# Optimization experiments

Hardware: AMD Instinct MI355X
Metric: run time of the kernel (lower is better)

The kernel has to match this reference:

```python
import jax, jax.numpy as jnp
import numpy as np

N = 100000
IN_C = 128
OUT_C = 200
E = 1600000


def gcn_conv(x, edge_index, W, b):
    """PyG GCNConv: symmetric degree-normalized aggregation with self-loops.
    out[v] = sum_{(u,v) in E+selfloops} d_u^-1/2 d_v^-1/2 (x_u @ W) + b
    """
    n = x.shape[0]
    xw = x @ W  # [N, out]
    loop = jnp.arange(n, dtype=edge_index.dtype)
    row = jnp.concatenate([edge_index[0], loop])  # src
    col = jnp.concatenate([edge_index[1], loop])  # dst
    ones = jnp.ones(row.shape[0], dtype=x.dtype)
    deg = jax.ops.segment_sum(ones, col, num_segments=n)  # in-degree incl. self
    dinv = jnp.where(deg > 0, jax.lax.rsqrt(deg), 0.0)
    norm = dinv[row] * dinv[col]  # [E+N]
    msgs = xw[row] * norm[:, None]  # [E+N, out]
    out = jax.ops.segment_sum(msgs, col, num_segments=n)
    return out + b


def setup_inputs() -> dict:
    key = jax.random.key(0)
    k1, k2, k3, k4 = jax.random.split(key, 4)
    x = jax.random.normal(k1, (N, IN_C), dtype=jnp.float32)
    edge_index = jax.random.randint(k2, (2, E), 0, N, dtype=jnp.int64)
    s1 = 1.0 / np.sqrt(IN_C)
    W1 = jax.random.uniform(k3, (IN_C, OUT_C), dtype=jnp.float32, minval=-s1, maxval=s1)
    b1 = jnp.zeros((OUT_C,), dtype=jnp.float32)
    W2 = jax.random.uniform(k4, (IN_C, OUT_C), dtype=jnp.float32, minval=-s1, maxval=s1)
    b2 = jnp.zeros((OUT_C,), dtype=jnp.float32)
    return {"x": x, "edge_index": edge_index, "W1": W1, "b1": b1, "W2": W2, "b2": b2}


def reference(x, edge_index, W1, b1, W2, b2):
    mu = gcn_conv(x, edge_index, W1, b1)
    logstd = gcn_conv(x, edge_index, W2, b2)
    return (mu, logstd)
```

## Files before the change

### kernel.cpp

```cpp
#include <hip/hip_runtime.h>

#define N_NODES 100000
#define IN_C    128
#define OUT_C   200
#define NT_TILES 13
#define KT_TILES 4

#define PSHIFT  8
#define NPB     256
#define NB      391
#define NB_POW2 512
#define BCAP    5120
#define PART_CH 4096
#define SEQ_P   16
#define SEQ_B   20

typedef __bf16 bf16_t;
typedef bf16_t bf16x8 __attribute__((ext_vector_type(8)));
typedef float  f32x4  __attribute__((ext_vector_type(4)));

__device__ __forceinline__ unsigned int bf16_bits(float f) {
    unsigned int u = __builtin_bit_cast(unsigned int, f);
    return (u + 0x7FFFu + ((u >> 16) & 1u)) >> 16;
}
__device__ __forceinline__ float bf16_lo(unsigned int p) {
    return __builtin_bit_cast(float, p << 16);
}
__device__ __forceinline__ float bf16_hi(unsigned int p) {
    return __builtin_bit_cast(float, p & 0xFFFF0000u);
}

__global__ __launch_bounds__(256) void partition_kernel(
        const int* __restrict__ row, const int* __restrict__ col, int E,
        int* __restrict__ gcount, unsigned int* __restrict__ gbuf) {
    __shared__ int hist[NB];
    __shared__ int base[NB];
    __shared__ int lofs[NB];
    __shared__ int pscan[256];
    __shared__ unsigned int stage[PART_CH];
    __shared__ unsigned short sb[PART_CH];
    const int tid = threadIdx.x;
    const int chunk = blockIdx.x * PART_CH;
    int cend = E - chunk; if (cend > PART_CH) cend = PART_CH;

    for (int i = tid; i < NB; i += 256) hist[i] = 0;
    __syncthreads();

    unsigned int   pay[SEQ_P];
    unsigned short eb[SEQ_P];
    unsigned short sq[SEQ_P];
    #pragma unroll
    for (int k = 0; k < SEQ_P; k++) {
        int i = tid + k * 256;
        eb[k] = 0xFFFFu;
        if (i < cend) {
            int c = col[chunk + i];
            int r = row[chunk + i];
            int b = (c >> PSHIFT) & (NB_POW2 - 1);
            if (b >= NB) b = NB - 1;
            pay[k] = (unsigned int)((c & (NPB - 1)) | (r << PSHIFT));
            eb[k]  = (unsigned short)b;
            sq[k]  = (unsigned short)atomicAdd(&hist[b], 1);
        }
    }
    __syncthreads();

    for (int i = tid; i < NB; i += 256)
        base[i] = atomicAdd(&gcount[i], hist[i]);

    int v0 = (2 * tid     < NB) ? hist[2 * tid]     : 0;
    int v1 = (2 * tid + 1 < NB) ? hist[2 * tid + 1] : 0;
    int s = v0 + v1;
    pscan[tid] = s;
    __syncthreads();
    for (int off = 1; off < 256; off <<= 1) {
        int u = (tid >= off) ? pscan[tid - off] : 0;
        __syncthreads();
        pscan[tid] += u;
        __syncthreads();
    }
    int ep = pscan[tid] - s;
    if (2 * tid     < NB) lofs[2 * tid]     = ep;
    if (2 * tid + 1 < NB) lofs[2 * tid + 1] = ep + v0;
    __syncthreads();

    #pragma unroll
    for (int k = 0; k < SEQ_P; k++) {
        if (eb[k] != 0xFFFFu) {
            int p = lofs[eb[k]] + sq[k];
            stage[p] = pay[k];
            sb[p] = eb[k];
        }
    }
    __syncthreads();

    for (int i = tid; i < cend; i += 256) {
        int b = sb[i];
        int p = base[b] + (i - lofs[b]);
        if (p < BCAP) gbuf[(size_t)b * BCAP + p] = stage[i];
    }
}

__global__ void bucket_scan_kernel(const int* __restrict__ gcount, int* __restrict__ gbase) {
    __shared__ int pscan[256];
    int tid = threadIdx.x;
    int v0 = (2 * tid     < NB) ? gcount[2 * tid]     : 0;
    int v1 = (2 * tid + 1 < NB) ? gcount[2 * tid + 1] : 0;
    if (v0 > BCAP) v0 = BCAP;
    if (v1 > BCAP) v1 = BCAP;
    int s = v0 + v1;
    pscan[tid] = s;
    __syncthreads();
    for (int off = 1; off < 256; off <<= 1) {
        int u = (tid >= off) ? pscan[tid - off] : 0;
        __syncthreads();
        pscan[tid] += u;
        __syncthreads();
    }
    int ep = pscan[tid] - s;
    if (2 * tid     < NB) gbase[2 * tid]     = ep;
    if (2 * tid + 1 < NB) gbase[2 * tid + 1] = ep + v0;
}

__global__ __launch_bounds__(256) void build_kernel(
        const unsigned int* __restrict__ gbuf, const int* __restrict__ gcount,
        const int* __restrict__ gbase, int* __restrict__ deg,
        int* __restrict__ offsets, float* __restrict__ dinv,
        int* __restrict__ csr_src, int n) {
    __shared__ int cnt[NPB];
    __shared__ int cur[NPB];
    __shared__ int pscan[256];
    const int b = blockIdx.x;
    const int tid = threadIdx.x;
    int total = gcount[b]; if (total > BCAP) total = BCAP;
    const int cbase = gbase[b];
    const unsigned int* bp = gbuf + (size_t)b * BCAP;

    cnt[tid] = 0;
    __syncthreads();

    unsigned int   ee[SEQ_B];
    unsigned short sq[SEQ_B];
    #pragma unroll
    for (int k = 0; k < SEQ_B; k++) {
        int i = tid + k * 256;
        ee[k] = 0xFFFFFFFFu;
        if (i < total) {
            unsigned int e = bp[i];
            ee[k] = e;
            sq[k] = (unsigned short)atomicAdd(&cnt[e & (NPB - 1)], 1);
        }
    }
    __syncthreads();

    int c = cnt[tid];
    pscan[tid] = c;
    __syncthreads();
    for (int off = 1; off < 256; off <<= 1) {
        int u = (tid >= off) ? pscan[tid - off] : 0;
        __syncthreads();
        pscan[tid] += u;
        __syncthreads();
    }
    int excl = pscan[tid] - c;
    cur[tid] = excl;
    int v = b * NPB + tid;
    if (v < n) {
        deg[v] = c;
        offsets[v] = cbase + excl;
        dinv[v] = rsqrtf((float)(c + 1));
    }
    __syncthreads();

    #pragma unroll
    for (int k = 0; k < SEQ_B; k++) {
        if (ee[k] != 0xFFFFFFFFu) {
            int p = cur[ee[k] & (NPB - 1)] + (int)sq[k];
            csr_src[cbase + p] = (int)(ee[k] >> PSHIFT);
        }
    }
}

__global__ void convert_xs_kernel(const float4* __restrict__ x, const float* __restrict__ dinv,
                                  uint2* __restrict__ xs4, int n) {
    int id = blockIdx.x * blockDim.x + threadIdx.x;
    if (id >= n * 32) return;
    int v = id >> 5;
    float dv = dinv[v];
    float4 f = x[id];
    uint2 o;
    o.x = bf16_bits(f.x * dv) | (bf16_bits(f.y * dv) << 16);
    o.y = bf16_bits(f.z * dv) | (bf16_bits(f.w * dv) << 16);
    xs4[id] = o;
}

__global__ __launch_bounds__(256) void gather_kernel(
        const uint2* __restrict__ xs4, const float* __restrict__ dinv,
        const int* __restrict__ offsets, const int* __restrict__ deg,
        const int* __restrict__ csr_src, uint2* __restrict__ agg4, int n) {
    int wave = threadIdx.x >> 6;
    int lane = threadIdx.x & 63;
    int half = lane >> 5;
    int hl   = lane & 31;
    int v = blockIdx.x * 4 + wave;
    if (v >= n) return;
    float dv = dinv[v];
    int start = offsets[v];
    int cnt = deg[v];
    float ax = 0.f, ay = 0.f, az = 0.f, aw = 0.f;

    const int* cp = csr_src + start;
    int i = 0;
    for (; i + 16 <= cnt; i += 16) {
        int u[8];
        #pragma unroll
        for (int j = 0; j < 8; j++) u[j] = __builtin_nontemporal_load(cp + i + 2 * j + half);
        uint2 t[8];
        #pragma unroll
        for (int j = 0; j < 8; j++) t[j] = xs4[(size_t)u[j] * 32 + hl];
        #pragma unroll
        for (int j = 0; j < 8; j++) {
            ax += bf16_lo(t[j].x); ay += bf16_hi(t[j].x);
            az += bf16_lo(t[j].y); aw += bf16_hi(t[j].y);
        }
    }
    if (i + 8 <= cnt) {
        int u[4];
        #pragma unroll
        for (int j = 0; j < 4; j++) u[j] = __builtin_nontemporal_load(cp + i + 2 * j + half);
        uint2 t[4];
        #pragma unroll
        for (int j = 0; j < 4; j++) t[j] = xs4[(size_t)u[j] * 32 + hl];
        #pragma unroll
        for (int j = 0; j < 4; j++) {
            ax += bf16_lo(t[j].x); ay += bf16_hi(t[j].x);
            az += bf16_lo(t[j].y); aw += bf16_hi(t[j].y);
        }
        i += 8;
    }
    if (i + 4 <= cnt) {
        int u[2];
        #pragma unroll
        for (int j = 0; j < 2; j++) u[j] = __builtin_nontemporal_load(cp + i + 2 * j + half);
        uint2 t[2];
        #pragma unroll
        for (int j = 0; j < 2; j++) t[j] = xs4[(size_t)u[j] * 32 + hl];
        #pragma unroll
        for (int j = 0; j < 2; j++) {
            ax += bf16_lo(t[j].x); ay += bf16_hi(t[j].x);
            az += bf16_lo(t[j].y); aw += bf16_hi(t[j].y);
        }
        i += 4;
    }
    if (i + 2 <= cnt) {
        int u = __builtin_nontemporal_load(cp + i + half);
        uint2 t = xs4[(size_t)u * 32 + hl];
        ax += bf16_lo(t.x); ay += bf16_hi(t.x);
        az += bf16_lo(t.y); aw += bf16_hi(t.y);
        i += 2;
    }
    if (i < cnt && half == 0) {
        int u = __builtin_nontemporal_load(cp + i);
        uint2 t = xs4[(size_t)u * 32 + hl];
        ax += bf16_lo(t.x); ay += bf16_hi(t.x);
        az += bf16_lo(t.y); aw += bf16_hi(t.y);
    }
    ax += __shfl_xor(ax, 32, 64);
    ay += __shfl_xor(ay, 32, 64);
    az += __shfl_xor(az, 32, 64);
    aw += __shfl_xor(aw, 32, 64);
    uint2 s = xs4[(size_t)v * 32 + hl];
    ax += bf16_lo(s.x); ay += bf16_hi(s.x);
    az += bf16_lo(s.y); aw += bf16_hi(s.y);
    if (half == 0) {
        uint2 o;
        o.x = bf16_bits(ax * dv) | (bf16_bits(ay * dv) << 16);
        o.y = bf16_bits(az * dv) | (bf16_bits(aw * dv) << 16);
        agg4[(size_t)v * 32 + hl] = o;
    }
}

__global__ void pack_w_kernel(const float* __restrict__ W1, const float* __restrict__ W2,
                              unsigned short* __restrict__ out) {
    int tid = blockIdx.x * blockDim.x + threadIdx.x;
    if (tid >= 2 * KT_TILES * NT_TILES * 64) return;
    int lane = tid & 63;
    int nt = (tid >> 6) % NT_TILES;
    int kt = (tid / (64 * NT_TILES)) % KT_TILES;
    int h  = tid / (64 * NT_TILES * KT_TILES);
    const float* W = h ? W2 : W1;
    int q = lane >> 4, r = lane & 15;
    int nn = nt * 16 + r;
    size_t dst = ((size_t)((nt * 2 + h) * KT_TILES + kt)) * 512 + (size_t)lane * 8;
    for (int j = 0; j < 8; j++) {
        int k = kt * 32 + q * 8 + j;
        float val = (nn < OUT_C) ? W[(size_t)k * OUT_C + nn] : 0.f;
        out[dst + j] = (unsigned short)bf16_bits(val);
    }
}

__global__ __launch_bounds__(256) void gemm_mfma_kernel(
        const unsigned short* __restrict__ agg,
        const unsigned short* __restrict__ Wpk,
        const float* __restrict__ b1, const float* __restrict__ b2,
        float* __restrict__ mu, float* __restrict__ ls, int M) {
    __shared__ uint4 Bs[2][512];
    int tid  = threadIdx.x;
    int wave = tid >> 6;
    int lane = tid & 63;
    int row0 = blockIdx.x * 64 + wave * 16;
    int q = lane >> 4, r = lane & 15;

    int arow = row0 + r; if (arow > M - 1) arow = M - 1;
    const unsigned short* ap = agg + (size_t)arow * IN_C + q * 8;
    bf16x8 afrag[KT_TILES];
    #pragma unroll
    for (int kt = 0; kt < KT_TILES; kt++) {
        uint4 u = *(const uint4*)(ap + kt * 32);
        afrag[kt] = __builtin_bit_cast(bf16x8, u);
    }

    f32x4 acc[2][NT_TILES];
    #pragma unroll
    for (int h = 0; h < 2; h++)
        #pragma unroll
        for (int nt = 0; nt < NT_TILES; nt++)
            acc[h][nt] = (f32x4){0.f, 0.f, 0.f, 0.f};

    const uint4* wsrc = (const uint4*)Wpk;
    uint4 pre0 = wsrc[tid];
    uint4 pre1 = wsrc[tid + 256];

    for (int nt = 0; nt < NT_TILES; nt++) {
        int buf = nt & 1;
        Bs[buf][tid]       = pre0;
        Bs[buf][tid + 256] = pre1;
        __syncthreads();
        if (nt + 1 < NT_TILES) {
            pre0 = wsrc[(nt + 1) * 512 + tid];
            pre1 = wsrc[(nt + 1) * 512 + tid + 256];
        }
        #pragma unroll
        for (int h = 0; h < 2; h++) {
            f32x4 c = acc[h][nt];
            #pragma unroll
            for (int kt = 0; kt < KT_TILES; kt++) {
                uint4 u = Bs[buf][(h * KT_TILES + kt) * 64 + lane];
                bf16x8 bfrag = __builtin_bit_cast(bf16x8, u);
                c = __builtin_amdgcn_mfma_f32_16x16x32_bf16(afrag[kt], bfrag, c, 0, 0, 0);
            }
            acc[h][nt] = c;
        }
    }

    float bv1r[NT_TILES], bv2r[NT_TILES];
    #pragma unroll
    for (int nt = 0; nt < NT_TILES; nt++) {
        int colx = nt * 16 + r;
        bool cok = colx < OUT_C;
        bv1r[nt] = cok ? b1[colx] : 0.f;
        bv2r[nt] = cok ? b2[colx] : 0.f;
    }
    #pragma unroll
    for (int reg = 0; reg < 4; reg++) {
        int gr = row0 + q * 4 + reg;
        if (gr < M) {
            float* mrow = mu + (size_t)gr * OUT_C;
            #pragma unroll
            for (int nt = 0; nt < NT_TILES; nt++) {
                int colx = nt * 16 + r;
                if (colx < OUT_C) mrow[colx] = acc[0][nt][reg] + bv1r[nt];
            }
            float* lrow = ls + (size_t)gr * OUT_C;
            #pragma unroll
            for (int nt = 0; nt < NT_TILES; nt++) {
                int colx = nt * 16 + r;
                if (colx < OUT_C) lrow[colx] = acc[1][nt][reg] + bv2r[nt];
            }
        }
    }
}

extern "C" void kernel_launch(void* const* d_in, const int* in_sizes, int n_in,
                              void* d_out, int out_size, void* d_ws, size_t ws_size,
                              hipStream_t stream) {
    const float* x  = (const float*)d_in[0];
    const int*   ei = (const int*)d_in[1];
    const float* W1 = (const float*)d_in[2];
    const float* b1 = (const float*)d_in[3];
    const float* W2 = (const float*)d_in[4];
    const float* b2 = (const float*)d_in[5];

    const int n = in_sizes[0] / IN_C;
    const int E = in_sizes[1] / 2;
    const int* row = ei;
    const int* col = ei + E;

    float* mu = (float*)d_out;
    float* ls = (float*)d_out + (size_t)n * OUT_C;

    char* ws = (char*)d_ws;
    int*            deg     = (int*)           (ws + 0);
    float*          dinv    = (float*)         (ws + 524288);
    int*            offsets = (int*)           (ws + 1048576);
    int*            gcount  = (int*)           (ws + 1572864);
    int*            gbase   = (int*)           (ws + 1576960);
    int*            csr_src = (int*)           (ws + 2162688);
    unsigned int*   xs2     = (unsigned int*)  (ws + 8562688);
    unsigned int*   gbuf    = (unsigned int*)  (ws + 34162688);
    unsigned int*   agg2    = (unsigned int*)  (ws + 42170368);
    unsigned short* Wpk     = (unsigned short*)(ws + 67770368);

    hipMemsetAsync(gcount, 0, NB * sizeof(int), stream);

    pack_w_kernel<<<(2 * KT_TILES * NT_TILES * 64 + 255) / 256, 256, 0, stream>>>(W1, W2, Wpk);

    partition_kernel<<<(E + PART_CH - 1) / PART_CH, 256, 0, stream>>>(row, col, E, gcount, gbuf);
    bucket_scan_kernel<<<1, 256, 0, stream>>>(gcount, gbase);
    build_kernel<<<NB, 256, 0, stream>>>(gbuf, gcount, gbase, deg, offsets, dinv, csr_src, n);

    convert_xs_kernel<<<(n * 32 + 255) / 256, 256, 0, stream>>>(
        (const float4*)x, dinv, (uint2*)xs2, n);

    gather_kernel<<<(n + 3) / 4, 256, 0, stream>>>(
        (const uint2*)xs2, dinv, offsets, deg, csr_src, (uint2*)agg2, n);

    gemm_mfma_kernel<<<(n + 63) / 64, 256, 0, stream>>>(
        (const unsigned short*)agg2, Wpk, b1, b2, mu, ls, n);
}
```

Baseline: 363.5 us.

## Fuse bucket scan and x conversion into build kernel, use nontemporal loads

Drops the single-block bucket scan kernel: every build block now computes the prefix scan over bucket counts itself. The x-to-bf16 conversion scaled by dinv moves into the build kernel too, each block converting its own 256 nodes using the in-shared degree counts. Edge and x reads become nontemporal loads. This removes two launches and the global round-trip of gbase and dinv, at the cost of every block repeating the redundant 391-element scan.

```diff
diff --git a/kernel.cpp b/kernel.cpp
--- a/kernel.cpp
+++ b/kernel.cpp
@@ -54,8 +54,8 @@
         int i = tid + k * 256;
         eb[k] = 0xFFFFu;
         if (i < cend) {
-            int c = col[chunk + i];
-            int r = row[chunk + i];
+            int c = __builtin_nontemporal_load(col + chunk + i);
+            int r = __builtin_nontemporal_load(row + chunk + i);
             int b = (c >> PSHIFT) & (NB_POW2 - 1);
             if (b >= NB) b = NB - 1;
             pay[k] = (unsigned int)((c & (NPB - 1)) | (r << PSHIFT));
@@ -101,43 +101,40 @@
     }
 }
 
-__global__ void bucket_scan_kernel(const int* __restrict__ gcount, int* __restrict__ gbase) {
-    __shared__ int pscan[256];
-    int tid = threadIdx.x;
-    int v0 = (2 * tid     < NB) ? gcount[2 * tid]     : 0;
-    int v1 = (2 * tid + 1 < NB) ? gcount[2 * tid + 1] : 0;
-    if (v0 > BCAP) v0 = BCAP;
-    if (v1 > BCAP) v1 = BCAP;
-    int s = v0 + v1;
-    pscan[tid] = s;
-    __syncthreads();
-    for (int off = 1; off < 256; off <<= 1) {
-        int u = (tid >= off) ? pscan[tid - off] : 0;
-        __syncthreads();
-        pscan[tid] += u;
-        __syncthreads();
-    }
-    int ep = pscan[tid] - s;
-    if (2 * tid     < NB) gbase[2 * tid]     = ep;
-    if (2 * tid + 1 < NB) gbase[2 * tid + 1] = ep + v0;
-}
-
 __global__ __launch_bounds__(256) void build_kernel(
         const unsigned int* __restrict__ gbuf, const int* __restrict__ gcount,
-        const int* __restrict__ gbase, int* __restrict__ deg,
-        int* __restrict__ offsets, float* __restrict__ dinv,
-        int* __restrict__ csr_src, int n) {
+        const float* __restrict__ x,
+        int* __restrict__ deg, int* __restrict__ offsets, float* __restrict__ dinv,
+        int* __restrict__ csr_src, uint2* __restrict__ xs4, int n) {
     __shared__ int cnt[NPB];
     __shared__ int cur[NPB];
     __shared__ int pscan[256];
+    __shared__ int gb[512];
     const int b = blockIdx.x;
     const int tid = threadIdx.x;
+
+    int g0 = (2 * tid     < NB) ? gcount[2 * tid]     : 0;
+    int g1 = (2 * tid + 1 < NB) ? gcount[2 * tid + 1] : 0;
+    if (g0 > BCAP) g0 = BCAP;
+    if (g1 > BCAP) g1 = BCAP;
+    int gs = g0 + g1;
+    pscan[tid] = gs;
+    cnt[tid] = 0;
+    __syncthreads();
+    for (int off = 1; off < 256; off <<= 1) {
+        int u = (tid >= off) ? pscan[tid - off] : 0;
+        __syncthreads();
+        pscan[tid] += u;
+        __syncthreads();
+    }
+    int gep = pscan[tid] - gs;
+    gb[2 * tid]     = gep;
+    gb[2 * tid + 1] = gep + g0;
+    __syncthreads();
+
+    const int cbase = gb[b];
     int total = gcount[b]; if (total > BCAP) total = BCAP;
-    const int cbase = gbase[b];
     const unsigned int* bp = gbuf + (size_t)b * BCAP;
-
-    cnt[tid] = 0;
-    __syncthreads();
 
     unsigned int   ee[SEQ_B];
     unsigned short sq[SEQ_B];
@@ -146,7 +143,7 @@
         int i = tid + k * 256;
         ee[k] = 0xFFFFFFFFu;
         if (i < total) {
-            unsigned int e = bp[i];
+            unsigned int e = __builtin_nontemporal_load(bp + i);
             ee[k] = e;
             sq[k] = (unsigned short)atomicAdd(&cnt[e & (NPB - 1)], 1);
         }
@@ -179,19 +176,21 @@
             csr_src[cbase + p] = (int)(ee[k] >> PSHIFT);
         }
     }
-}
-
-__global__ void convert_xs_kernel(const float4* __restrict__ x, const float* __restrict__ dinv,
-                                  uint2* __restrict__ xs4, int n) {
-    int id = blockIdx.x * blockDim.x + threadIdx.x;
-    if (id >= n * 32) return;
-    int v = id >> 5;
-    float dv = dinv[v];
-    float4 f = x[id];
-    uint2 o;
-    o.x = bf16_bits(f.x * dv) | (bf16_bits(f.y * dv) << 16);
-    o.y = bf16_bits(f.z * dv) | (bf16_bits(f.w * dv) << 16);
-    xs4[id] = o;
+
+    int wv = tid >> 6, ln = tid & 63;
+    int hlf = ln >> 5, hl2 = ln & 31;
+    for (int m = 0; m < 64; m += 2) {
+        int local = wv * 64 + m + hlf;
+        int nv = b * NPB + local;
+        if (nv < n) {
+            float dv = rsqrtf((float)(cnt[local] + 1));
+            f32x4 f = __builtin_nontemporal_load((const f32x4*)x + (size_t)nv * 32 + hl2);
+            uint2 o;
+            o.x = bf16_bits(f.x * dv) | (bf16_bits(f.y * dv) << 16);
+            o.y = bf16_bits(f.z * dv) | (bf16_bits(f.w * dv) << 16);
+            xs4[(size_t)nv * 32 + hl2] = o;
+        }
+    }
 }
 
 __global__ __launch_bounds__(256) void gather_kernel(
@@ -404,23 +403,20 @@
     float*          dinv    = (float*)         (ws + 524288);
     int*            offsets = (int*)           (ws + 1048576);
     int*            gcount  = (int*)           (ws + 1572864);
-    int*            gbase   = (int*)           (ws + 1576960);
     int*            csr_src = (int*)           (ws + 2162688);
     unsigned int*   xs2     = (unsigned int*)  (ws + 8562688);
     unsigned int*   gbuf    = (unsigned int*)  (ws + 34162688);
     unsigned int*   agg2    = (unsigned int*)  (ws + 42170368);
     unsigned short* Wpk     = (unsigned short*)(ws + 67770368);
 
-    hipMemsetAsync(gcount, 0, NB * sizeof(int), stream);
+    (void)hipMemsetAsync(gcount, 0, NB * sizeof(int), stream);
 
     pack_w_kernel<<<(2 * KT_TILES * NT_TILES * 64 + 255) / 256, 256, 0, stream>>>(W1, W2, Wpk);
 
     partition_kernel<<<(E + PART_CH - 1) / PART_CH, 256, 0, stream>>>(row, col, E, gcount, gbuf);
-    bucket_scan_kernel<<<1, 256, 0, stream>>>(gcount, gbase);
-    build_kernel<<<NB, 256, 0, stream>>>(gbuf, gcount, gbase, deg, offsets, dinv, csr_src, n);
-
-    convert_xs_kernel<<<(n * 32 + 255) / 256, 256, 0, stream>>>(
-        (const float4*)x, dinv, (uint2*)xs2, n);
+
+    build_kernel<<<NB, 256, 0, stream>>>(gbuf, gcount, x, deg, offsets, dinv,
+                                         csr_src, (uint2*)xs2, n);
 
     gather_kernel<<<(n + 3) / 4, 256, 0, stream>>>(
         (const uint2*)xs2, dinv, offsets, deg, csr_src, (uint2*)agg2, n);
```

After: 364.5 us. Within noise of the previous version (+0.3%).
